# Performance work log

Hardware: AMD Instinct MI355X
Metric: run time of the kernel (lower is better)

Reference implementation:

```python
import jax, jax.numpy as jnp
import numpy as np

NEG = -10000.0
PAD_ID = 0


def setup_inputs() -> dict:
    key = jax.random.key(0)
    ks = jax.random.split(key, 9)
    B, S, D, K, L = 32, 256, 512, 8, 64
    word_rep = jax.random.normal(ks[0], (B, S, D), jnp.float32)
    mask = jnp.ones((B, S), jnp.int32)
    # conv_w[k,:,:,:k+1] are the taps of Conv1d(D, D, k+1); padded to width K for a single tensor
    conv_w = jax.random.normal(ks[1], (K, D, D, K), jnp.float32) * 0.02
    conv_b = jax.random.normal(ks[2], (K, D), jnp.float32) * 0.02
    cls_w = jax.random.normal(ks[3], (L, D), jnp.float32) * 0.02
    cls_b = jax.random.normal(ks[4], (L,), jnp.float32) * 0.02
    T = jax.random.normal(ks[5], (L, L), jnp.float32) * 0.01
    T = T.at[PAD_ID, :].set(NEG).at[:, PAD_ID].set(NEG)
    T_from_BEGIN = jax.random.normal(ks[6], (L,), jnp.float32) * 0.01
    T_from_BEGIN = T_from_BEGIN.at[PAD_ID].set(NEG)
    T_to_END = jax.random.normal(ks[7], (L,), jnp.float32) * 0.01
    T_to_END = T_to_END.at[PAD_ID].set(NEG)
    return dict(word_rep=word_rep, mask=mask, conv_w=conv_w, conv_b=conv_b,
                cls_w=cls_w, cls_b=cls_b, T=T, T_from_BEGIN=T_from_BEGIN, T_to_END=T_to_END)


def _semicrf(word_rep, mask, conv_w, conv_b, cls_w, cls_b, T, T_from_BEGIN, T_to_END):
    B, S, D = word_rep.shape
    K = conv_w.shape[0]
    L = cls_w.shape[0]
    # ---- segment representations: Conv1d(D, D, k+1) placed at [:, k:, k, :] ----
    x = jnp.transpose(word_rep, (0, 2, 1))  # [B, D, S]
    word_seq_rep = jnp.zeros((B, S, K, D), word_rep.dtype)
    for k in range(K):
        w = conv_w[k, :, :, :k + 1]  # [D_out, D_in, k+1]
        out = jax.lax.conv_general_dilated(
            x, w, window_strides=(1,), padding='VALID',
            dimension_numbers=('NCH', 'OIH', 'NCH')) + conv_b[k][None, :, None]  # [B, D, S-k]
        word_seq_rep = word_seq_rep.at[:, k:, k, :].set(jnp.transpose(out, (0, 2, 1)))
    # ---- label scores ----
    label_score = jnp.einsum('bskd,ld->bskl', word_seq_rep, cls_w) + cls_b  # [B,S,K,L]
    label_score = label_score.at[..., PAD_ID].set(NEG)
    seg_ok = jnp.arange(K)[None, :] <= jnp.arange(S)[:, None]  # [S, K]: segment of len k+1 valid only if t >= k
    mask3 = (mask[:, :, None] == 1) & seg_ok[None]              # [B, S, K]
    label_score = jnp.where(mask3[..., None], label_score, NEG)
    # ---- semi-CRF forward recursion over t (sequential scan) ----
    # buf[:, j] holds log_alpha at position t-1-j for j in [0, K)
    def step(buf, inp):
        ls_t, m_t, t = inp  # [B,K,L], [B,K], scalar
        lse_prev = jax.nn.logsumexp(buf, axis=2)                                  # over kk -> [B,K,L']
        tmp = jax.nn.logsumexp(T[None, None, :, :] + lse_prev[:, :, None, :], axis=3)  # over l' -> [B,K,L]
        rec = jnp.where(m_t[..., None], ls_t + tmp, NEG)
        begin = ls_t + T_from_BEGIN[None, None, :]
        karr = jnp.arange(K)[None, :, None]
        row = jnp.where(karr == t, begin, jnp.where(karr > t, NEG, rec))  # [B,K,L]
        buf = jnp.concatenate([row[:, None], buf[:, :-1]], axis=1)
        return buf, row

    buf0 = jnp.full((B, K, K, L), NEG, word_rep.dtype)
    xs = (jnp.transpose(label_score, (1, 0, 2, 3)), jnp.transpose(mask3, (1, 0, 2)), jnp.arange(S))
    _, rows = jax.lax.scan(step, buf0, xs)
    log_alpha = jnp.concatenate(
        [jnp.transpose(rows, (1, 0, 2, 3)), jnp.full((B, 1, K, L), NEG, word_rep.dtype)], axis=1)  # [B,S+1,K,L]
    # ---- log partition: gather log_alpha at last token per segment length, add T_to_END, logsumexp ----
    lengths = jnp.sum(mask, axis=1)                                   # [B]
    idxs = lengths[:, None] - (jnp.arange(K)[None, :] + 1)            # [B,K]
    idxs = jnp.where(idxs >= 0, idxs, S - 1)
    idx_arr = jnp.broadcast_to(idxs[:, None, :, None], (B, 1, K, L))
    g = jnp.take_along_axis(log_alpha, idx_arr, axis=1)[:, 0]         # [B,K,L]
    scores = g + T_to_END[None, None, :]
    return jax.nn.logsumexp(scores.reshape(B, K * L), axis=1)         # [B]


def reference(word_rep, mask, conv_w, conv_b, cls_w, cls_b, T, T_from_BEGIN, T_to_END):
    return _semicrf(word_rep, mask, conv_w, conv_b, cls_w, cls_b, T, T_from_BEGIN, T_to_END)
```

## Files before the change

kernel.cpp:

```cpp
#include <hip/hip_runtime.h>
#include <hip/hip_bf16.h>

#define NEGV (-10000.0f)
constexpr int B_ = 32, S_ = 256, D_ = 512, K_ = 8, L_ = 64;

typedef __bf16 bf16_t;
typedef bf16_t bf16x8 __attribute__((ext_vector_type(8)));
typedef float f32x4 __attribute__((ext_vector_type(4)));

__device__ __forceinline__ float u2f(unsigned int u) {
  union { unsigned int u; float f; } x; x.u = u; return x.f;
}
__device__ __forceinline__ unsigned int f2bfbits(float f) {
  union { bf16_t h; unsigned short u; } x; x.h = (bf16_t)f; return (unsigned int)x.u;
}

__global__ __launch_bounds__(256) void cast_kernel(const float* __restrict__ wr,
                                                   bf16_t* __restrict__ Awr,
                                                   const float* __restrict__ cls_w,
                                                   bf16_t* __restrict__ clsb) {
  const int bid = blockIdx.x;
  if (bid < 2048) {
    const int i = (bid * 256 + threadIdx.x) * 8;
    const float4 a = *(const float4*)(wr + i);
    const float4 b = *(const float4*)(wr + i + 4);
    bf16x8 o;
    o[0] = (bf16_t)a.x; o[1] = (bf16_t)a.y; o[2] = (bf16_t)a.z; o[3] = (bf16_t)a.w;
    o[4] = (bf16_t)b.x; o[5] = (bf16_t)b.y; o[6] = (bf16_t)b.z; o[7] = (bf16_t)b.w;
    *(bf16x8*)(Awr + i) = o;
  } else {
    const int i = ((bid - 2048) * 256 + threadIdx.x) * 8;
    const float4 a = *(const float4*)(cls_w + i);
    const float4 b = *(const float4*)(cls_w + i + 4);
    bf16x8 o;
    o[0] = (bf16_t)a.x; o[1] = (bf16_t)a.y; o[2] = (bf16_t)a.z; o[3] = (bf16_t)a.w;
    o[4] = (bf16_t)b.x; o[5] = (bf16_t)b.y; o[6] = (bf16_t)b.z; o[7] = (bf16_t)b.w;
    *(bf16x8*)(clsb + i) = o;
  }
}

__global__ __launch_bounds__(256) void w2_kernel(const float* __restrict__ conv_w,
                                                 const bf16_t* __restrict__ clsb,
                                                 bf16_t* __restrict__ Vt,
                                                 const float* __restrict__ conv_b,
                                                 const float* __restrict__ cls_w,
                                                 const float* __restrict__ cls_b,
                                                 float* __restrict__ bias2) {
  const int k = blockIdx.y;
  const int m0 = blockIdx.x * 128;
  const int tid = threadIdx.x;
  const int w = tid >> 6, lane = tid & 63;
  const int wm = w & 1, wn = w >> 1;
  const int lrow = lane & 15, quad = lane >> 4;
  const float* A = conv_w + (size_t)k * 2097152;
  f32x4 acc[4][2] = {};
#pragma unroll 2
  for (int kk = 0; kk < 16; kk++) {
    const int d0 = kk * 32 + quad * 8;
    const bf16x8 b0 = *(const bf16x8*)(clsb + (wn * 32 + lrow) * 512 + kk * 32 + quad * 8);
    const bf16x8 b1 = *(const bf16x8*)(clsb + (wn * 32 + 16 + lrow) * 512 + kk * 32 + quad * 8);
#pragma unroll
    for (int mi = 0; mi < 4; mi++) {
      const int ih = m0 + wm * 64 + mi * 16 + lrow;
      const float* ap = A + (size_t)d0 * 4096 + ih;
      bf16x8 a;
      a[0] = (bf16_t)ap[0 * 4096]; a[1] = (bf16_t)ap[1 * 4096];
      a[2] = (bf16_t)ap[2 * 4096]; a[3] = (bf16_t)ap[3 * 4096];
      a[4] = (bf16_t)ap[4 * 4096]; a[5] = (bf16_t)ap[5 * 4096];
      a[6] = (bf16_t)ap[6 * 4096]; a[7] = (bf16_t)ap[7 * 4096];
      acc[mi][0] = __builtin_amdgcn_mfma_f32_16x16x32_bf16(a, b0, acc[mi][0], 0, 0, 0);
      acc[mi][1] = __builtin_amdgcn_mfma_f32_16x16x32_bf16(a, b1, acc[mi][1], 0, 0, 0);
    }
  }
#pragma unroll
  for (int mi = 0; mi < 4; mi++) {
#pragma unroll
    for (int dd = 0; dd < 4; dd++) {
      const int ih = m0 + wm * 64 + mi * 16 + quad * 4 + dd;
      const int i = ih >> 3, h = ih & 7;
      const int o = k - h;
      if (o >= 0) {
#pragma unroll
        for (int ni = 0; ni < 2; ni++) {
          const int l = wn * 32 + ni * 16 + lrow;
          Vt[(size_t)(k * 64 + l) * 4096 + o * 512 + i] = (bf16_t)acc[mi][ni][dd];
        }
      }
    }
  }
  if (blockIdx.x == 0) {
    __shared__ float partb[4][64];
    const int bl = tid & 63, bc = tid >> 6;
    float s = 0.f;
    for (int d = bc * 128; d < bc * 128 + 128; d++)
      s += conv_b[k * D_ + d] * cls_w[bl * D_ + d];
    partb[bc][bl] = s;
    __syncthreads();
    if (tid < 64)
      bias2[k * 64 + tid] = cls_b[tid] + partb[0][tid] + partb[1][tid] + partb[2][tid] + partb[3][tid];
  }
}

__global__ __launch_bounds__(256) void ls_mfma(const bf16_t* __restrict__ Awr,
                                               const bf16_t* __restrict__ Vt,
                                               const float* __restrict__ bias2,
                                               const int* __restrict__ mask,
                                               unsigned int* __restrict__ ELSd) {
  constexpr int LDA = 520;
  __shared__ __align__(16) bf16_t As[71 * LDA];
  const int tid = threadIdx.x;
  const int m0 = blockIdx.x * 64;
  const int y = blockIdx.y;
  const int w = tid >> 6, lane = tid & 63;
  const int lrow = lane & 15, quad = lane >> 4;
  const int tblA[4] = {7, 0, 5, 2}, tblB[4] = {6, 1, 4, 3};
  const int kS = (y == 0) ? tblA[w] : tblB[w];

  for (int c = tid; c < 71 * 64; c += 256) {
    const int row = c >> 6, col8 = c & 63;
    int src = m0 - 7 + row;
    if (src < 0) src = 0;
    const uint4 v = *(const uint4*)(Awr + (size_t)src * 512 + col8 * 8);
    *(uint4*)(&As[row * LDA + col8 * 8]) = v;
  }
  __syncthreads();

  f32x4 acc[4][4] = {};
  const int NJ = 16 * (kS + 1);
  const bf16_t* vbase = Vt + (size_t)(kS * 64 + lrow) * 4096 + quad * 8;
#pragma unroll 2
  for (int j = 0; j < NJ; j++) {
    const int o = j >> 4;
    const int col = (j & 15) * 32;
    bf16x8 bfr[4];
#pragma unroll
    for (int ni = 0; ni < 4; ni++)
      bfr[ni] = *(const bf16x8*)(vbase + (size_t)(ni * 16) * 4096 + j * 32);
    const int abase = (lrow + 7 - o) * LDA + col + quad * 8;
#pragma unroll
    for (int mi = 0; mi < 4; mi++) {
      const bf16x8 a = *(const bf16x8*)(&As[abase + mi * 16 * LDA]);
#pragma unroll
      for (int ni = 0; ni < 4; ni++)
        acc[mi][ni] = __builtin_amdgcn_mfma_f32_16x16x32_bf16(a, bfr[ni], acc[mi][ni], 0, 0, 0);
    }
  }

  __syncthreads();
  unsigned short* buf = (unsigned short*)As;
#pragma unroll
  for (int ni = 0; ni < 4; ni++) {
    const int l = ni * 16 + lrow;
    const float bn = bias2[kS * 64 + l];
#pragma unroll
    for (int mi = 0; mi < 4; mi++) {
#pragma unroll
      for (int d = 0; d < 4; d++) {
        const int ml = mi * 16 + quad * 4 + d;
        const int m = m0 + ml;
        const int t = m & 255;
        const bool mok = (mask[m] == 1) && (t >= kS) && (l != 0);
        const float e = mok ? __expf(acc[mi][ni][d] + bn) : 0.f;
        buf[w * 4096 + ml * 64 + l] = (unsigned short)f2bfbits(e);
      }
    }
  }
  __syncthreads();
#pragma unroll
  for (int g = 0; g < 2; g++) {
    const int plane = g * 2 + y;
    const unsigned short* lo = buf + (g * 2) * 4096;
    const unsigned short* hi = buf + (g * 2 + 1) * 4096;
#pragma unroll
    for (int it = 0; it < 16; it++) {
      const int idx = it * 256 + tid;
      const unsigned int dw = (unsigned int)lo[idx] | ((unsigned int)hi[idx] << 16);
      ELSd[((size_t)plane * 8192 + m0 + (idx >> 6)) * 64 + (idx & 63)] = dw;
    }
  }
}

__global__ __launch_bounds__(64) void dp_kernel(const float* __restrict__ T,
                                                const float* __restrict__ Tfb_g,
                                                const unsigned int* __restrict__ ELSd,
                                                float* __restrict__ Mg_lin,
                                                float* __restrict__ cs_g) {
  const int b = blockIdx.x;
  const int l = threadIdx.x;
  __shared__ __align__(16) float ebuf[64];

  f32x4 rTv[16];
#pragma unroll
  for (int jj = 0; jj < 16; jj++) {
    const float4 tv = *(const float4*)(T + l * 64 + jj * 4);
    rTv[jj][0] = __expf(tv.x);
    rTv[jj][1] = __expf(tv.y);
    rTv[jj][2] = __expf(tv.z);
    rTv[jj][3] = __expf(tv.w);
  }

  const unsigned int* e0p = ELSd + ((size_t)0 * 8192 + b * 256) * 64 + l;
  const unsigned int* e1p = ELSd + ((size_t)1 * 8192 + b * 256) * 64 + l;
  const unsigned int* e2p = ELSd + ((size_t)2 * 8192 + b * 256) * 64 + l;
  const unsigned int* e3p = ELSd + ((size_t)3 * 8192 + b * 256) * 64 + l;

  float mh0 = __expf(Tfb_g[l]);
  float mh1 = 0.f, mh2 = 0.f, mh3 = 0.f, mh4 = 0.f, mh5 = 0.f, mh6 = 0.f, mh7 = 0.f;
  float c = 0.f;
  float m4 = 0.f;
  float S_next = 0.f;

  uint4 r0 = make_uint4(e0p[0 * 64], e1p[0 * 64], e2p[0 * 64], e3p[0 * 64]);
  uint4 r1 = make_uint4(e0p[1 * 64], e1p[1 * 64], e2p[1 * 64], e3p[1 * 64]);
  uint4 r2 = make_uint4(e0p[2 * 64], e1p[2 * 64], e2p[2 * 64], e3p[2 * 64]);
  uint4 r3 = make_uint4(e0p[3 * 64], e1p[3 * 64], e2p[3 * 64], e3p[3 * 64]);

  float e = u2f(r0.x & 0xFFFF0000u) * mh0;

#define DP_STEP(U, RQ, RN)                                                      \
  {                                                                             \
    const int t = t4 + (U);                                                     \
    ebuf[l] = e;                                                                \
                    \
    const float nf7 = u2f(RN.x << 16), nk0 = u2f(RN.x & 0xFFFF0000u);           \
    const float nf6 = u2f(RN.y << 16), nk1 = u2f(RN.y & 0xFFFF0000u);           \
    const float nf5 = u2f(RN.z << 16), nk2 = u2f(RN.z & 0xFFFF0000u);           \
    const float nf4 = u2f(RN.w << 16), nk3 = u2f(RN.w & 0xFFFF0000u);           \
    const float pe = ((nk1 * mh0 + nk2 * mh1) + (nk3 * mh2 + nf4 * mh3)) +      \
                     ((nf5 * mh4 + nf6 * mh5) + nf7 * mh6);                     \
                                                  \
    {                                                                           \
      int nt = t + 4; if (nt > 255) nt = 255;                                   \
      RQ = make_uint4(e0p[(size_t)nt * 64], e1p[(size_t)nt * 64],               \
                      e2p[(size_t)nt * 64], e3p[(size_t)nt * 64]);              \
    }                                                                           \
                                     \
    const f32x4* ev = (const f32x4*)ebuf;                                       \
    f32x4 A0 = {0.f, 0.f, 0.f, 0.f}, A1 = {0.f, 0.f, 0.f, 0.f};                 \
    f32x4 A2 = {0.f, 0.f, 0.f, 0.f}, A3 = {0.f, 0.f, 0.f, 0.f};                 \
    if ((U) == 3) {                                                             \
      f32x4 s0 = {0.f, 0.f, 0.f, 0.f}, s1 = {0.f, 0.f, 0.f, 0.f};               \
      _Pragma("unroll")                                                         \
      for (int jj = 0; jj < 4; jj++) {                                          \
        const f32x4 v0 = ev[jj], v1 = ev[4 + jj], v2 = ev[8 + jj], v3 = ev[12 + jj]; \
        A0 += rTv[jj] * v0; A1 += rTv[4 + jj] * v1;                             \
        A2 += rTv[8 + jj] * v2; A3 += rTv[12 + jj] * v3;                        \
        s0 += v0 + v2; s1 += v1 + v3;                                           \
      }                                                                         \
      const f32x4 ss = s0 + s1;                                                 \
      S_next = (ss[0] + ss[1]) + (ss[2] + ss[3]);                               \
    } else {                                                                    \
      _Pragma("unroll")                                                         \
      for (int jj = 0; jj < 4; jj++) {                                          \
        A0 += rTv[jj] * ev[jj]; A1 += rTv[4 + jj] * ev[4 + jj];                 \
        A2 += rTv[8 + jj] * ev[8 + jj]; A3 += rTv[12 + jj] * ev[12 + jj];       \
      }                                                                         \
    }                                                                           \
    const f32x4 As4 = (A0 + A1) + (A2 + A3);                                    \
    m4 = (As4[0] + As4[1]) + (As4[2] + As4[3]);                                 \
    Mg_lin[((size_t)b * 256 + t) * 64 + l] = m4;                                \
    if (l == 0) cs_g[b * 256 + t] = c;                                          \
     \
    if ((U) == 3) {                                                             \
      const float S = fmaxf(S_next, 1e-30f);                                    \
      const float inv = __builtin_amdgcn_rcpf(S);                               \
      c += __logf(S);                                                           \
      mh7 = mh6 * inv; mh6 = mh5 * inv; mh5 = mh4 * inv; mh4 = mh3 * inv;       \
      mh3 = mh2 * inv; mh2 = mh1 * inv; mh1 = mh0 * inv; mh0 = m4 * inv;        \
      e = inv * (nk0 * m4 + pe);                                                \
    } else {                                                                    \
      mh7 = mh6; mh6 = mh5; mh5 = mh4; mh4 = mh3;                               \
      mh3 = mh2; mh2 = mh1; mh1 = mh0; mh0 = m4;                                \
      e = nk0 * m4 + pe;                                                        \
    }                                                                           \
  }

  for (int t4 = 0; t4 < 256; t4 += 4) {
    DP_STEP(0, r0, r1)
    DP_STEP(1, r1, r2)
    DP_STEP(2, r2, r3)
    DP_STEP(3, r3, r0)
  }
#undef DP_STEP
}

__global__ __launch_bounds__(64) void final_kernel(const int* __restrict__ mask,
                                                   const float* __restrict__ Tfb_g,
                                                   const float* __restrict__ T2e_g,
                                                   const unsigned int* __restrict__ ELSd,
                                                   const float* __restrict__ Mg_lin,
                                                   const float* __restrict__ cs_g,
                                                   float* __restrict__ out) {
  const int b = blockIdx.x, lane = threadIdx.x;
  int lenp = 0;
  for (int s = lane; s < S_; s += 64) lenp += (mask[b * S_ + s] == 1) ? 1 : 0;
#pragma unroll
  for (int off = 32; off > 0; off >>= 1) lenp += __shfl_xor(lenp, off);
  const int len = lenp;
  const float t2e = T2e_g[lane];
  float vals[8];
  float mx = -3.4e38f;
#pragma unroll
  for (int k = 0; k < 8; k++) {
    int tk = len - 1 - k;
    if (tk < 0) tk = S_ - 1;
    float g;
    if (k > tk) {
      g = NEGV;
    } else {
      const int p = (k < 4) ? k : (7 - k);
      const unsigned int dw = ELSd[((size_t)p * 8192 + b * 256 + tk) * 64 + lane];
      const float elsv = (k < 4) ? u2f(dw & 0xFFFF0000u) : u2f(dw << 16);
      const float ls = (elsv > 0.f) ? __logf(elsv) : NEGV;
      if (k == tk) {
        g = ls + Tfb_g[lane];
      } else if (mask[b * S_ + tk] == 1) {
        const int u = tk - 1 - k;
        const float mlin = Mg_lin[((size_t)b * S_ + u) * 64 + lane];
        const float M = (mlin > 0.f) ? (__logf(mlin) + cs_g[b * S_ + u]) : -1e30f;
        g = ls + M;
      } else {
        g = NEGV;
      }
    }
    const float v = g + t2e;
    vals[k] = v;
    mx = fmaxf(mx, v);
  }
#pragma unroll
  for (int off = 32; off > 0; off >>= 1) mx = fmaxf(mx, __shfl_xor(mx, off));
  float s = 0.f;
#pragma unroll
  for (int k = 0; k < 8; k++) s += __expf(vals[k] - mx);
#pragma unroll
  for (int off = 32; off > 0; off >>= 1) s += __shfl_xor(s, off);
  if (lane == 0) out[b] = __logf(s) + mx;
}

extern "C" void kernel_launch(void* const* d_in, const int* in_sizes, int n_in,
                              void* d_out, int out_size, void* d_ws, size_t ws_size,
                              hipStream_t stream) {
  const float* wr     = (const float*)d_in[0];
  const int*   mask   = (const int*)d_in[1];
  const float* conv_w = (const float*)d_in[2];
  const float* conv_b = (const float*)d_in[3];
  const float* cls_w  = (const float*)d_in[4];
  const float* cls_b  = (const float*)d_in[5];
  const float* T      = (const float*)d_in[6];
  const float* Tfb    = (const float*)d_in[7];
  const float* T2e    = (const float*)d_in[8];
  float* out = (float*)d_out;

  float* ws = (float*)d_ws;
  bf16_t* Vt    = (bf16_t*)ws;
  bf16_t* Awr   = (bf16_t*)(ws + 1048576);
  float*  bias2 = ws + 3145728;
  unsigned int* ELSd = (unsigned int*)(ws + 3146240);
  float*  Mg    = ws + 5243392;
  float*  cs    = ws + 5767680;
  bf16_t* clsb  = (bf16_t*)(ws + 5775872);

  cast_kernel<<<2064, 256, 0, stream>>>(wr, Awr, cls_w, clsb);
  w2_kernel<<<dim3(32, 8), 256, 0, stream>>>(conv_w, clsb, Vt, conv_b, cls_w, cls_b, bias2);
  ls_mfma<<<dim3(128, 2), 256, 0, stream>>>(Awr, Vt, bias2, mask, ELSd);
  dp_kernel<<<32, 64, 0, stream>>>(T, Tfb, ELSd, Mg, cs);
  final_kernel<<<32, 64, 0, stream>>>(mask, Tfb, T2e, ELSd, Mg, cs, out);
}
```

Baseline: 288.0 us.

## Restructure ls_mfma into 32-row tiles with two balanced k-passes per wave

The label-score MFMA kernel now gives each block 32 rows instead of 64 and launches 256 one-dimensional blocks instead of a 128x2 grid. Each wave handles segment lengths 7-w and w in two passes, so the work per wave is balanced. The two bf16 results are packed into a dword in registers and written straight to global memory, which removes the LDS staging buffer and its extra syncs. The trade-offs are more re-reads of the 7-row A halo and of Vt across blocks, smaller MFMA tiles per B-fragment load, and uncoalesced 4-byte global stores strided by l.

Measured after the change: 290.5 us. About the same (+0.9%).

```diff
diff --git a/kernel.cpp b/kernel.cpp
--- a/kernel.cpp
+++ b/kernel.cpp
@@ -107,16 +107,13 @@
                                                const int* __restrict__ mask,
                                                unsigned int* __restrict__ ELSd) {
   constexpr int LDA = 520;
-  __shared__ __align__(16) bf16_t As[71 * LDA];
+  __shared__ __align__(16) bf16_t As[39 * LDA];
   const int tid = threadIdx.x;
-  const int m0 = blockIdx.x * 64;
-  const int y = blockIdx.y;
+  const int m0 = blockIdx.x * 32;
   const int w = tid >> 6, lane = tid & 63;
   const int lrow = lane & 15, quad = lane >> 4;
-  const int tblA[4] = {7, 0, 5, 2}, tblB[4] = {6, 1, 4, 3};
-  const int kS = (y == 0) ? tblA[w] : tblB[w];
-
-  for (int c = tid; c < 71 * 64; c += 256) {
+
+  for (int c = tid; c < 39 * 64; c += 256) {
     const int row = c >> 6, col8 = c & 63;
     int src = m0 - 7 + row;
     if (src < 0) src = 0;
@@ -125,57 +122,50 @@
   }
   __syncthreads();
 
-  f32x4 acc[4][4] = {};
-  const int NJ = 16 * (kS + 1);
-  const bf16_t* vbase = Vt + (size_t)(kS * 64 + lrow) * 4096 + quad * 8;
-#pragma unroll 2
-  for (int j = 0; j < NJ; j++) {
-    const int o = j >> 4;
-    const int col = (j & 15) * 32;
-    bf16x8 bfr[4];
-#pragma unroll
-    for (int ni = 0; ni < 4; ni++)
-      bfr[ni] = *(const bf16x8*)(vbase + (size_t)(ni * 16) * 4096 + j * 32);
-    const int abase = (lrow + 7 - o) * LDA + col + quad * 8;
-#pragma unroll
-    for (int mi = 0; mi < 4; mi++) {
-      const bf16x8 a = *(const bf16x8*)(&As[abase + mi * 16 * LDA]);
+  unsigned int eaLo[2][4][4];
+
+#pragma unroll
+  for (int pass = 0; pass < 2; pass++) {
+    const int kS = (pass == 0) ? (7 - w) : w;
+    const int NJ = 16 * (kS + 1);
+    f32x4 acc[2][4] = {};
+    const bf16_t* vbase = Vt + (size_t)(kS * 64 + lrow) * 4096 + quad * 8;
+    for (int j = 0; j < NJ; j++) {
+      const int o = j >> 4;
+      const int col = (j & 15) * 32;
+      bf16x8 bfr[4];
 #pragma unroll
       for (int ni = 0; ni < 4; ni++)
-        acc[mi][ni] = __builtin_amdgcn_mfma_f32_16x16x32_bf16(a, bfr[ni], acc[mi][ni], 0, 0, 0);
-    }
-  }
-
-  __syncthreads();
-  unsigned short* buf = (unsigned short*)As;
-#pragma unroll
-  for (int ni = 0; ni < 4; ni++) {
-    const int l = ni * 16 + lrow;
-    const float bn = bias2[kS * 64 + l];
-#pragma unroll
-    for (int mi = 0; mi < 4; mi++) {
-#pragma unroll
-      for (int d = 0; d < 4; d++) {
-        const int ml = mi * 16 + quad * 4 + d;
-        const int m = m0 + ml;
-        const int t = m & 255;
-        const bool mok = (mask[m] == 1) && (t >= kS) && (l != 0);
-        const float e = mok ? __expf(acc[mi][ni][d] + bn) : 0.f;
-        buf[w * 4096 + ml * 64 + l] = (unsigned short)f2bfbits(e);
+        bfr[ni] = *(const bf16x8*)(vbase + (size_t)(ni * 16) * 4096 + j * 32);
+      const int abase = (lrow + 7 - o) * LDA + col + quad * 8;
+#pragma unroll
+      for (int mi = 0; mi < 2; mi++) {
+        const bf16x8 a = *(const bf16x8*)(&As[abase + mi * 16 * LDA]);
+#pragma unroll
+        for (int ni = 0; ni < 4; ni++)
+          acc[mi][ni] = __builtin_amdgcn_mfma_f32_16x16x32_bf16(a, bfr[ni], acc[mi][ni], 0, 0, 0);
       }
     }
-  }
-  __syncthreads();
-#pragma unroll
-  for (int g = 0; g < 2; g++) {
-    const int plane = g * 2 + y;
-    const unsigned short* lo = buf + (g * 2) * 4096;
-    const unsigned short* hi = buf + (g * 2 + 1) * 4096;
-#pragma unroll
-    for (int it = 0; it < 16; it++) {
-      const int idx = it * 256 + tid;
-      const unsigned int dw = (unsigned int)lo[idx] | ((unsigned int)hi[idx] << 16);
-      ELSd[((size_t)plane * 8192 + m0 + (idx >> 6)) * 64 + (idx & 63)] = dw;
+#pragma unroll
+    for (int mi = 0; mi < 2; mi++) {
+#pragma unroll
+      for (int ni = 0; ni < 4; ni++) {
+        const int l = ni * 16 + lrow;
+        const float bn = bias2[kS * 64 + l];
+#pragma unroll
+        for (int d = 0; d < 4; d++) {
+          const int m = m0 + mi * 16 + quad * 4 + d;
+          const int t = m & 255;
+          const bool mok = (mask[m] == 1) && (t >= kS) && (l != 0);
+          const float e = mok ? __expf(acc[mi][ni][d] + bn) : 0.f;
+          if (pass == 0) {
+            eaLo[mi][ni][d] = f2bfbits(e);
+          } else {
+            const unsigned int dw = eaLo[mi][ni][d] | (f2bfbits(e) << 16);
+            ELSd[((size_t)w * 8192 + m) * 64 + l] = dw;
+          }
+        }
+      }
     }
   }
 }
@@ -260,7 +250,6 @@
     m4 = (As4[0] + As4[1]) + (As4[2] + As4[3]);                                 \
     Mg_lin[((size_t)b * 256 + t) * 64 + l] = m4;                                \
     if (l == 0) cs_g[b * 256 + t] = c;                                          \
-     \
     if ((U) == 3) {                                                             \
       const float S = fmaxf(S_next, 1e-30f);                                    \
       const float inv = __builtin_amdgcn_rcpf(S);                               \
@@ -362,7 +351,7 @@
 
   cast_kernel<<<2064, 256, 0, stream>>>(wr, Awr, cls_w, clsb);
   w2_kernel<<<dim3(32, 8), 256, 0, stream>>>(conv_w, clsb, Vt, conv_b, cls_w, cls_b, bias2);
-  ls_mfma<<<dim3(128, 2), 256, 0, stream>>>(Awr, Vt, bias2, mask, ELSd);
+  ls_mfma<<<256, 256, 0, stream>>>(Awr, Vt, bias2, mask, ELSd);
   dp_kernel<<<32, 64, 0, stream>>>(T, Tfb, ELSd, Mg, cs);
   final_kernel<<<32, 64, 0, stream>>>(mask, Tfb, T2e, ELSd, Mg, cs, out);
 }
```
